# Kernel tuning notes

Hardware: AMD Instinct MI355X
Metric: run time of the kernel (lower is better)

The kernel has to match this reference:

```python
import jax, jax.numpy as jnp
import numpy as np
import math

D_MODEL = 2048
HEADS = 16
D_K = D_MODEL // HEADS  # 128
D_FF = 2048
N = 8192
EPS = 1e-6


def _norm(x, alpha, bias):
    # torch Norm: alpha * (x - mean) / (std + eps) + bias, std uses ddof=1
    mu = jnp.mean(x, axis=-1, keepdims=True)
    sd = jnp.std(x, axis=-1, ddof=1, keepdims=True)
    return alpha * (x - mu) / (sd + EPS) + bias


def setup_inputs() -> dict:
    key = jax.random.key(0)
    ks = jax.random.split(key, 16)
    s = 0.02
    inp = {
        "q": jax.random.normal(ks[0], (N, D_MODEL), jnp.float32),
        "k": jax.random.normal(ks[1], (N, D_MODEL), jnp.float32),
        "v": jax.random.normal(ks[2], (N, D_MODEL), jnp.float32),
        # norm params (norm_1 exists in module but is unused in forward)
        "nq_a": jnp.ones((D_MODEL,), jnp.float32), "nq_b": jnp.zeros((D_MODEL,), jnp.float32),
        "nk_a": jnp.ones((D_MODEL,), jnp.float32), "nk_b": jnp.zeros((D_MODEL,), jnp.float32),
        "nv_a": jnp.ones((D_MODEL,), jnp.float32), "nv_b": jnp.zeros((D_MODEL,), jnp.float32),
        "n2_a": jnp.ones((D_MODEL,), jnp.float32), "n2_b": jnp.zeros((D_MODEL,), jnp.float32),
        # attention projections, stored [in, out]
        "Wq": jax.random.normal(ks[3], (D_MODEL, D_MODEL), jnp.float32) * s,
        "bq": jnp.zeros((D_MODEL,), jnp.float32),
        "Wk": jax.random.normal(ks[4], (D_MODEL, D_MODEL), jnp.float32) * s,
        "bk": jnp.zeros((D_MODEL,), jnp.float32),
        "Wv": jax.random.normal(ks[5], (D_MODEL, D_MODEL), jnp.float32) * s,
        "bv": jnp.zeros((D_MODEL,), jnp.float32),
        "Wo": jax.random.normal(ks[6], (D_MODEL, D_MODEL), jnp.float32) * s,
        "bo": jnp.zeros((D_MODEL,), jnp.float32),
        # FFN
        "W1": jax.random.normal(ks[7], (D_MODEL, D_FF), jnp.float32) * s,
        "b1": jnp.zeros((D_FF,), jnp.float32),
        "W2": jax.random.normal(ks[8], (D_FF, D_MODEL), jnp.float32) * s,
        "b2": jnp.zeros((D_MODEL,), jnp.float32),
    }
    return inp


def reference(q, k, v,
              nq_a, nq_b, nk_a, nk_b, nv_a, nv_b, n2_a, n2_b,
              Wq, bq, Wk, bk, Wv, bv, Wo, bo, W1, b1, W2, b2):
    x = v  # residual stream (dropout is identity at inference)
    qn = _norm(q, nq_a, nq_b)
    kn = _norm(k, nk_a, nk_b)
    vn = _norm(v, nv_a, nv_b)

    # projections -> [N, h, d_k] then transpose(1,2) -> [N, d_k, h]
    qh = (qn @ Wq + bq).reshape(N, HEADS, D_K).transpose(0, 2, 1)
    kh = (kn @ Wk + bk).reshape(N, HEADS, D_K).transpose(0, 2, 1)
    vh = (vn @ Wv + bv).reshape(N, HEADS, D_K).transpose(0, 2, 1)

    # NON-STANDARD (as-written in source): per-token [d_k, d_k] attention
    # contracting over the head axis, scaled by 1/sqrt(d_k).
    scores = jnp.einsum('nah,nbh->nab', qh, kh) / math.sqrt(D_K)  # [N, d_k, d_k]
    probs = jax.nn.softmax(scores, axis=-1)
    attn = jnp.einsum('nab,nbh->nah', probs, vh)  # [N, d_k, h]

    concat = attn.transpose(0, 2, 1).reshape(N, D_MODEL)  # [N, h*d_k]
    x = x + (concat @ Wo + bo)

    x2 = _norm(x, n2_a, n2_b)
    ff = jax.nn.relu(x2 @ W1 + b1) @ W2 + b2
    return x + ff
```

## Files before the change

### kernel.cpp

```cpp
#include <hip/hip_runtime.h>
#include <hip/hip_bf16.h>

#define DM 2048
#define NTOK 8192
#define EPS 1e-6f

typedef __attribute__((ext_vector_type(8))) short short8;
typedef __attribute__((ext_vector_type(4))) short short4v;
typedef __attribute__((ext_vector_type(4))) float f32x4;
typedef __attribute__((ext_vector_type(16))) float f32x16;
typedef __attribute__((ext_vector_type(4))) unsigned int u32x4;

typedef const __attribute__((address_space(1))) void gvoid;
typedef __attribute__((address_space(3))) void lvoid;

static __device__ __forceinline__ unsigned short f2bf(float f) {
    unsigned u = __builtin_bit_cast(unsigned, f);
    unsigned r = u + 0x7FFFu + ((u >> 16) & 1u);
    return (unsigned short)(r >> 16);
}
static __device__ __forceinline__ float bf2f(unsigned short h) {
    return __builtin_bit_cast(float, (unsigned)h << 16);
}

__global__ __launch_bounds__(256) void norm_rows(
        const float* __restrict__ in, const float* __restrict__ alpha,
        const float* __restrict__ beta, unsigned short* __restrict__ out) {
    const int row = blockIdx.x;
    const int t = threadIdx.x;
    const float* x = in + (size_t)row * DM + t * 8;
    float4 v0 = *(const float4*)(x);
    float4 v1 = *(const float4*)(x + 4);
    float s = (v0.x + v0.y) + (v0.z + v0.w) + (v1.x + v1.y) + (v1.z + v1.w);
    float ss = v0.x*v0.x + v0.y*v0.y + v0.z*v0.z + v0.w*v0.w
             + v1.x*v1.x + v1.y*v1.y + v1.z*v1.z + v1.w*v1.w;
    #pragma unroll
    for (int m = 1; m < 64; m <<= 1) {
        s  += __shfl_xor(s, m);
        ss += __shfl_xor(ss, m);
    }
    __shared__ float red[8];
    const int wv = t >> 6, ln = t & 63;
    if (ln == 0) { red[wv] = s; red[4 + wv] = ss; }
    __syncthreads();
    s  = (red[0] + red[1]) + (red[2] + red[3]);
    ss = (red[4] + red[5]) + (red[6] + red[7]);
    const float mu = s * (1.0f / DM);
    float var = (ss - s * mu) * (1.0f / (DM - 1));
    var = fmaxf(var, 0.0f);
    const float scale = 1.0f / (sqrtf(var) + EPS);
    float4 a0 = *(const float4*)(alpha + t*8);
    float4 a1 = *(const float4*)(alpha + t*8 + 4);
    float4 b0 = *(const float4*)(beta + t*8);
    float4 b1 = *(const float4*)(beta + t*8 + 4);
    short8 o;
    o[0] = (short)f2bf(a0.x * (v0.x - mu) * scale + b0.x);
    o[1] = (short)f2bf(a0.y * (v0.y - mu) * scale + b0.y);
    o[2] = (short)f2bf(a0.z * (v0.z - mu) * scale + b0.z);
    o[3] = (short)f2bf(a0.w * (v0.w - mu) * scale + b0.w);
    o[4] = (short)f2bf(a1.x * (v1.x - mu) * scale + b1.x);
    o[5] = (short)f2bf(a1.y * (v1.y - mu) * scale + b1.y);
    o[6] = (short)f2bf(a1.z * (v1.z - mu) * scale + b1.z);
    o[7] = (short)f2bf(a1.w * (v1.w - mu) * scale + b1.w);
    *(short8*)(out + (size_t)row * DM + t * 8) = o;
}

__global__ __launch_bounds__(256) void norm_rows_bf16(
        const unsigned short* __restrict__ in, const float* __restrict__ alpha,
        const float* __restrict__ beta, unsigned short* __restrict__ out) {
    const int row = blockIdx.x;
    const int t = threadIdx.x;
    short8 rv = *(const short8*)(in + (size_t)row * DM + t * 8);
    float xv[8];
    #pragma unroll
    for (int j = 0; j < 8; ++j) xv[j] = bf2f((unsigned short)rv[j]);
    float s = 0.f, ss = 0.f;
    #pragma unroll
    for (int j = 0; j < 8; ++j) { s += xv[j]; ss += xv[j]*xv[j]; }
    #pragma unroll
    for (int m = 1; m < 64; m <<= 1) {
        s  += __shfl_xor(s, m);
        ss += __shfl_xor(ss, m);
    }
    __shared__ float red[8];
    const int wv = t >> 6, ln = t & 63;
    if (ln == 0) { red[wv] = s; red[4 + wv] = ss; }
    __syncthreads();
    s  = (red[0] + red[1]) + (red[2] + red[3]);
    ss = (red[4] + red[5]) + (red[6] + red[7]);
    const float mu = s * (1.0f / DM);
    float var = (ss - s * mu) * (1.0f / (DM - 1));
    var = fmaxf(var, 0.0f);
    const float scale = 1.0f / (sqrtf(var) + EPS);
    short8 o;
    #pragma unroll
    for (int j = 0; j < 8; ++j) {
        const float av = alpha[t*8 + j], bv = beta[t*8 + j];
        o[j] = (short)f2bf(av * (xv[j] - mu) * scale + bv);
    }
    *(short8*)(out + (size_t)row * DM + t * 8) = o;
}

__global__ __launch_bounds__(256) void wtrans(
        const float* __restrict__ W, unsigned short* __restrict__ Wt, int perm, float wscale) {
    __shared__ float tile[32][33];
    const int bc = blockIdx.x * 32, bk = blockIdx.y * 32;
    const int t = threadIdx.x;
    const int tc = t & 31, tr = t >> 5;
    #pragma unroll
    for (int i = 0; i < 4; ++i)
        tile[tr + i*8][tc] = W[(size_t)(bk + tr + i*8) * DM + bc + tc];
    __syncthreads();
    #pragma unroll
    for (int i = 0; i < 4; ++i) {
        const int c = bc + tr + i*8;
        const int pc = perm ? ((c & 127) * 16 + (c >> 7)) : c;
        Wt[(size_t)pc * DM + bk + tc] = f2bf(tile[tc][tr + i*8] * wscale);
    }
}

#define BARRIER __builtin_amdgcn_s_barrier()
#define WAIT_LGKM0 asm volatile("s_waitcnt lgkmcnt(0)" ::: "memory")
#define VMCNT(n) asm volatile("s_waitcnt vmcnt(" #n ")" ::: "memory")

template<int EPI>
__global__ __launch_bounds__(512, 2) void gemm256(
        const unsigned short* __restrict__ A, const unsigned short* __restrict__ Bt,
        const float* __restrict__ bias, const float* __restrict__ residF,
        const unsigned short* __restrict__ residB,
        float* __restrict__ outF, unsigned short* __restrict__ outB, int biasPerm,
        float bscale) {
    __shared__ __align__(16) char lds[131072];
    char* ldsA = lds;
    char* ldsB = lds + 65536;

    const int t = threadIdx.x, l = t & 63, w = t >> 6;
    const int wm = w >> 2, wn = w & 3;

    const int b = blockIdx.x;
    const int xcd = b & 7;
    const int j = b >> 3;
    const int m0 = (xcd * 4 + (j & 3)) * 256;
    const int n0 = (j >> 2) * 256;

    const int rS = t >> 3;
    const int cS = ((t & 7) ^ (rS & 7)) * 8;
    const unsigned short* aSt = A  + (size_t)(m0 + rS) * 2048 + cS;
    const unsigned short* bSt = Bt + (size_t)(n0 + rS) * 2048 + cS;
    const int ldsStW = w * 1024;

    const int aRd = wm * 16384 + (l & 15) * 128;
    const int bRd = (wn >> 1) * 16384 + (wn & 1) * 8192 + (l & 15) * 128;
    const int ch0 = (((l >> 4) + 0) ^ (l & 7)) * 16;
    const int ch1 = (((l >> 4) + 4) ^ (l & 7)) * 16;

    short8 af[4][2], bf[4][2];
    f32x4 acc[8][4] = {};

#define STG_A(buf, h, kt) do { \
    __builtin_amdgcn_global_load_lds((gvoid*)(aSt + (size_t)((h)*128)*2048 + (kt)*64), \
        (lvoid*)(ldsA + (buf)*32768 + (h)*16384 + ldsStW), 16, 0, 0); \
    __builtin_amdgcn_global_load_lds((gvoid*)(aSt + (size_t)((h)*128+64)*2048 + (kt)*64), \
        (lvoid*)(ldsA + (buf)*32768 + (h)*16384 + 8192 + ldsStW), 16, 0, 0); \
} while(0)
#define STG_B(buf, h, kt) do { \
    __builtin_amdgcn_global_load_lds((gvoid*)(bSt + (size_t)((h)*128)*2048 + (kt)*64), \
        (lvoid*)(ldsB + (buf)*32768 + (h)*16384 + ldsStW), 16, 0, 0); \
    __builtin_amdgcn_global_load_lds((gvoid*)(bSt + (size_t)((h)*128+64)*2048 + (kt)*64), \
        (lvoid*)(ldsB + (buf)*32768 + (h)*16384 + 8192 + ldsStW), 16, 0, 0); \
} while(0)
#define RD_A(buf, mh) do { \
    _Pragma("unroll") for (int ml = 0; ml < 4; ++ml) { \
        af[ml][0] = *(const short8*)(ldsA + (buf)*32768 + aRd + ((mh)*4+ml)*2048 + ch0); \
        af[ml][1] = *(const short8*)(ldsA + (buf)*32768 + aRd + ((mh)*4+ml)*2048 + ch1); \
    } } while(0)
#define RD_B(buf, nh) do { \
    _Pragma("unroll") for (int nl = 0; nl < 2; ++nl) { \
        bf[(nh)*2+nl][0] = *(const short8*)(ldsB + (buf)*32768 + bRd + ((nh)*2+nl)*2048 + ch0); \
        bf[(nh)*2+nl][1] = *(const short8*)(ldsB + (buf)*32768 + bRd + ((nh)*2+nl)*2048 + ch1); \
    } } while(0)
#define MM_Q(mh, nh) do { \
    __builtin_amdgcn_s_setprio(1); \
    _Pragma("unroll") for (int ml = 0; ml < 4; ++ml) \
    _Pragma("unroll") for (int nl = 0; nl < 2; ++nl) { \
        acc[(mh)*4+ml][(nh)*2+nl] = __builtin_amdgcn_mfma_f32_16x16x32_bf16( \
            af[ml][0], bf[(nh)*2+nl][0], acc[(mh)*4+ml][(nh)*2+nl], 0, 0, 0); \
        acc[(mh)*4+ml][(nh)*2+nl] = __builtin_amdgcn_mfma_f32_16x16x32_bf16( \
            af[ml][1], bf[(nh)*2+nl][1], acc[(mh)*4+ml][(nh)*2+nl], 0, 0, 0); \
    } \
    __builtin_amdgcn_s_setprio(0); \
} while(0)

    STG_B(0, 0, 0); STG_B(0, 1, 0); STG_A(0, 0, 0); STG_A(0, 1, 0);
    STG_B(1, 0, 1); STG_B(1, 1, 1);
    VMCNT(4);
    BARRIER;

    #pragma unroll 1
    for (int i = 0; i < 16; ++i) {
        const int kt1 = 2*i + 1, k2 = 2*i + 2, k3 = 2*i + 3;
        const bool more = (i < 15);
        RD_A(0, 0); RD_B(0, 0);
        STG_A(1, 0, kt1);
        BARRIER; WAIT_LGKM0;
        MM_Q(0, 0);
        BARRIER;
        RD_B(0, 1);
        STG_A(1, 1, kt1);
        BARRIER; WAIT_LGKM0;
        MM_Q(0, 1);
        BARRIER;
        RD_A(0, 1);
        if (more) STG_B(0, 0, k2);
        BARRIER; WAIT_LGKM0;
        MM_Q(1, 1);
        BARRIER;
        if (more) { STG_B(0, 1, k2); VMCNT(4); } else { VMCNT(0); }
        BARRIER;
        MM_Q(1, 0);
        BARRIER;
        RD_A(1, 0); RD_B(1, 0);
        if (more) STG_A(0, 0, k2);
        BARRIER; WAIT_LGKM0;
        MM_Q(0, 0);
        BARRIER;
        RD_B(1, 1);
        if (more) STG_A(0, 1, k2);
        BARRIER; WAIT_LGKM0;
        MM_Q(0, 1);
        BARRIER;
        RD_A(1, 1);
        if (more) STG_B(1, 0, k3);
        BARRIER; WAIT_LGKM0;
        MM_Q(1, 1);
        BARRIER;
        if (more) { STG_B(1, 1, k3); VMCNT(4); }
        BARRIER;
        MM_Q(1, 0);
        BARRIER;
    }

    #pragma unroll
    for (int ni = 0; ni < 4; ++ni) {
        const int col = n0 + wn*64 + ni*16 + (l & 15);
        const int cb = biasPerm ? ((col >> 4) + (col & 15) * 128) : col;
        const float bvv = bias[cb] * bscale;
        #pragma unroll
        for (int mi = 0; mi < 8; ++mi) {
            #pragma unroll
            for (int r = 0; r < 4; ++r) {
                const int rowg = m0 + wm*128 + mi*16 + (l >> 4)*4 + r;
                float vv = acc[mi][ni][r] + bvv;
                if (EPI == 1) vv = fmaxf(vv, 0.0f);
                const size_t idx = (size_t)rowg * 2048 + col;
                if (EPI == 3)      outB[idx] = f2bf(vv + residF[idx]);
                else if (EPI == 4) outF[idx] = vv + bf2f(residB[idx]);
                else               outB[idx] = f2bf(vv);
            }
        }
    }
#undef STG_A
#undef STG_B
#undef RD_A
#undef RD_B
#undef MM_Q
}

__global__ __launch_bounds__(256) void attn_tok(
        const unsigned short* __restrict__ Qt, const unsigned short* __restrict__ Kt,
        const unsigned short* __restrict__ Vp, unsigned short* __restrict__ Cc) {
    const int n = blockIdx.x;
    const int t = threadIdx.x, w = t >> 6, l = t & 63;
    const int q31 = l & 31, hi = l >> 5;
    __shared__ __align__(16) unsigned short c_s[16 * 132];

    const size_t tb = (size_t)n * DM;
    const short8 qf = *(const short8*)(Qt + tb + (w*32 + q31)*16 + hi*8);
    short8 kf[4];
    #pragma unroll
    for (int bt = 0; bt < 4; ++bt)
        kf[bt] = *(const short8*)(Kt + tb + (bt*32 + q31)*16 + hi*8);
    short8 vf[8];
    #pragma unroll
    for (int ks = 0; ks < 8; ++ks)
        vf[ks] = *(const short8*)(Vp + tb + (q31 & 15)*128 + ks*16 + hi*8);

    const f32x16 z = {};
    f32x16 sc[4];
    #pragma unroll
    for (int bt = 0; bt < 4; ++bt)
        sc[bt] = __builtin_amdgcn_mfma_f32_32x32x16_bf16(kf[bt], qf, z, 0, 0, 0);

    float m0 = sc[0][0], m1 = sc[1][0], m2 = sc[2][0], m3 = sc[3][0];
    #pragma unroll
    for (int r = 1; r < 16; ++r) {
        m0 = fmaxf(m0, sc[0][r]); m1 = fmaxf(m1, sc[1][r]);
        m2 = fmaxf(m2, sc[2][r]); m3 = fmaxf(m3, sc[3][r]);
    }
    float mx = fmaxf(fmaxf(m0, m1), fmaxf(m2, m3));
    { float a2 = mx, b2 = mx;
      asm volatile("v_permlane32_swap_b32 %0, %1" : "+v"(a2), "+v"(b2));
      mx = fmaxf(a2, b2); }

    float p[4][16];
    float s0 = 0.f, s1 = 0.f, s2 = 0.f, s3 = 0.f;
    #pragma unroll
    for (int r = 0; r < 16; ++r) {
        p[0][r] = __expf(sc[0][r] - mx); s0 += p[0][r];
        p[1][r] = __expf(sc[1][r] - mx); s1 += p[1][r];
        p[2][r] = __expf(sc[2][r] - mx); s2 += p[2][r];
        p[3][r] = __expf(sc[3][r] - mx); s3 += p[3][r];
    }
    float sm = (s0 + s1) + (s2 + s3);
    { float a2 = sm, b2 = sm;
      asm volatile("v_permlane32_swap_b32 %0, %1" : "+v"(a2), "+v"(b2));
      sm = a2 + b2; }
    const float inv = __builtin_amdgcn_rcpf(sm);
    #pragma unroll
    for (int bt = 0; bt < 4; ++bt)
        #pragma unroll
        for (int r = 0; r < 16; ++r)
            p[bt][r] *= inv;

    f32x16 acc = {};
    #pragma unroll
    for (int ks = 0; ks < 8; ++ks) {
        const int bt = ks >> 1, r0 = (ks & 1) * 8;
        unsigned X0, Y0, X1, Y1;
        asm("v_cvt_pk_bf16_f32 %0, %1, %2" : "=v"(X0) : "v"(p[bt][r0+0]), "v"(p[bt][r0+1]));
        asm("v_cvt_pk_bf16_f32 %0, %1, %2" : "=v"(Y0) : "v"(p[bt][r0+4]), "v"(p[bt][r0+5]));
        asm("v_cvt_pk_bf16_f32 %0, %1, %2" : "=v"(X1) : "v"(p[bt][r0+2]), "v"(p[bt][r0+3]));
        asm("v_cvt_pk_bf16_f32 %0, %1, %2" : "=v"(Y1) : "v"(p[bt][r0+6]), "v"(p[bt][r0+7]));
        asm volatile("v_permlane32_swap_b32 %0, %1" : "+v"(X0), "+v"(Y0));
        asm volatile("v_permlane32_swap_b32 %0, %1" : "+v"(X1), "+v"(Y1));
        u32x4 pw; pw[0] = X0; pw[1] = X1; pw[2] = Y0; pw[3] = Y1;
        const short8 paf = __builtin_bit_cast(short8, pw);
        acc = __builtin_amdgcn_mfma_f32_32x32x16_bf16(paf, vf[ks], acc, 0, 0, 0);
    }

    if (q31 < 16) {
        #pragma unroll
        for (int rp = 0; rp < 8; ++rp) {
            const int r = rp * 2;
            const int a = (r & 3) + 8 * (r >> 2) + 4 * hi;
            unsigned pk;
            asm("v_cvt_pk_bf16_f32 %0, %1, %2" : "=v"(pk) : "v"(acc[r]), "v"(acc[r+1]));
            *(unsigned*)((char*)c_s + q31*264 + (w*32 + a)*2) = pk;
        }
    }
    __syncthreads();
    *(short8*)(Cc + tb + t*8) = *(const short8*)((char*)c_s + (t >> 4)*264 + (t & 15)*16);
}

extern "C" void kernel_launch(void* const* d_in, const int* in_sizes, int n_in,
                              void* d_out, int out_size, void* d_ws, size_t ws_size,
                              hipStream_t stream) {
    (void)in_sizes; (void)n_in; (void)out_size; (void)ws_size;
    const float* q    = (const float*)d_in[0];
    const float* k    = (const float*)d_in[1];
    const float* v    = (const float*)d_in[2];
    const float* nq_a = (const float*)d_in[3];
    const float* nq_b = (const float*)d_in[4];
    const float* nk_a = (const float*)d_in[5];
    const float* nk_b = (const float*)d_in[6];
    const float* nv_a = (const float*)d_in[7];
    const float* nv_b = (const float*)d_in[8];
    const float* n2_a = (const float*)d_in[9];
    const float* n2_b = (const float*)d_in[10];
    const float* Wq   = (const float*)d_in[11];
    const float* bq   = (const float*)d_in[12];
    const float* Wk   = (const float*)d_in[13];
    const float* bk   = (const float*)d_in[14];
    const float* Wv   = (const float*)d_in[15];
    const float* bv   = (const float*)d_in[16];
    const float* Wo   = (const float*)d_in[17];
    const float* bo   = (const float*)d_in[18];
    const float* W1   = (const float*)d_in[19];
    const float* b1   = (const float*)d_in[20];
    const float* W2   = (const float*)d_in[21];
    const float* b2   = (const float*)d_in[22];

    char* ws = (char*)d_ws;
    const size_t MB = 1024 * 1024;
    unsigned short* buf0 = (unsigned short*)(ws);
    unsigned short* QtB  = (unsigned short*)(ws + 32*MB);
    unsigned short* KtB  = (unsigned short*)(ws + 64*MB);
    unsigned short* VpB  = (unsigned short*)(ws + 96*MB);
    unsigned short* Wqt  = (unsigned short*)(ws + 128*MB);
    unsigned short* Wkt  = (unsigned short*)(ws + 136*MB);
    unsigned short* Wvt  = (unsigned short*)(ws + 144*MB);
    unsigned short* Wot  = (unsigned short*)(ws + 152*MB);
    unsigned short* W1t  = (unsigned short*)(ws + 160*MB);
    unsigned short* W2t  = (unsigned short*)(ws + 168*MB);
    unsigned short* x2   = QtB;
    unsigned short* h1   = KtB;
    unsigned short* xb   = VpB;
    float* x = (float*)d_out;

    const float isq = 0.088388347648318447f;

    dim3 b256(256);
    dim3 gT(DM / 32, DM / 32);
    wtrans<<<gT, b256, 0, stream>>>(Wq, Wqt, 1, isq);
    wtrans<<<gT, b256, 0, stream>>>(Wk, Wkt, 1, 1.0f);
    wtrans<<<gT, b256, 0, stream>>>(Wv, Wvt, 0, 1.0f);
    wtrans<<<gT, b256, 0, stream>>>(Wo, Wot, 0, 1.0f);
    wtrans<<<gT, b256, 0, stream>>>(W1, W1t, 0, 1.0f);
    wtrans<<<gT, b256, 0, stream>>>(W2, W2t, 0, 1.0f);

    dim3 gN(NTOK);
    dim3 gG(256);
    dim3 b512(512);

    norm_rows<<<gN, b256, 0, stream>>>(q, nq_a, nq_b, buf0);
    gemm256<0><<<gG, b512, 0, stream>>>(buf0, Wqt, bq, nullptr, nullptr, nullptr, QtB, 1, isq);
    norm_rows<<<gN, b256, 0, stream>>>(k, nk_a, nk_b, buf0);
    gemm256<0><<<gG, b512, 0, stream>>>(buf0, Wkt, bk, nullptr, nullptr, nullptr, KtB, 1, 1.0f);
    norm_rows<<<gN, b256, 0, stream>>>(v, nv_a, nv_b, buf0);
    gemm256<0><<<gG, b512, 0, stream>>>(buf0, Wvt, bv, nullptr, nullptr, nullptr, VpB, 0, 1.0f);
    attn_tok<<<gN, b256, 0, stream>>>(QtB, KtB, VpB, buf0);
    gemm256<3><<<gG, b512, 0, stream>>>(buf0, Wot, bo, v, nullptr, nullptr, xb, 0, 1.0f);
    norm_rows_bf16<<<gN, b256, 0, stream>>>(xb, n2_a, n2_b, x2);
    gemm256<1><<<gG, b512, 0, stream>>>(x2, W1t, b1, nullptr, nullptr, nullptr, h1, 0, 1.0f);
    gemm256<4><<<gG, b512, 0, stream>>>(h1, W2t, b2, nullptr, xb, x, nullptr, 0, 1.0f);
}
```

Before: 598.8 us.

## Stage GEMM epilogue through LDS, restructure prefetch, batch weight transposes

The GEMM epilogue now writes bias-added bf16 results into LDS in two passes, then reads them back as 16-byte row segments for coalesced vector global stores and residual loads. Scalar per-element stores spread across strided rows go away. The K-loop prefetch now issues a whole A/B stage up front and groups the stage loads differently, waiting on a deeper vmcnt. The six weight-transpose launches are merged into one launch using blockIdx.z. The tradeoff is extra LDS round trips and barriers in the epilogue, plus an intermediate bf16 rounding before the residual add.

```diff
diff --git a/kernel.cpp b/kernel.cpp
--- a/kernel.cpp
+++ b/kernel.cpp
@@ -101,9 +101,20 @@
     *(short8*)(out + (size_t)row * DM + t * 8) = o;
 }
 
-__global__ __launch_bounds__(256) void wtrans(
-        const float* __restrict__ W, unsigned short* __restrict__ Wt, int perm, float wscale) {
+__global__ __launch_bounds__(256) void wtrans6(
+        const float* __restrict__ Wq, const float* __restrict__ Wk,
+        const float* __restrict__ Wv, const float* __restrict__ Wo,
+        const float* __restrict__ W1, const float* __restrict__ W2,
+        unsigned short* __restrict__ Tq, unsigned short* __restrict__ Tk,
+        unsigned short* __restrict__ Tv, unsigned short* __restrict__ To,
+        unsigned short* __restrict__ T1, unsigned short* __restrict__ T2,
+        float isq) {
     __shared__ float tile[32][33];
+    const int z = blockIdx.z;
+    const float* W = z==0?Wq: z==1?Wk: z==2?Wv: z==3?Wo: z==4?W1: W2;
+    unsigned short* Wt = z==0?Tq: z==1?Tk: z==2?Tv: z==3?To: z==4?T1: T2;
+    const int perm = (z < 2) ? 1 : 0;
+    const float ws = (z == 0) ? isq : 1.0f;
     const int bc = blockIdx.x * 32, bk = blockIdx.y * 32;
     const int t = threadIdx.x;
     const int tc = t & 31, tr = t >> 5;
@@ -115,7 +126,7 @@
     for (int i = 0; i < 4; ++i) {
         const int c = bc + tr + i*8;
         const int pc = perm ? ((c & 127) * 16 + (c >> 7)) : c;
-        Wt[(size_t)pc * DM + bk + tc] = f2bf(tile[tc][tr + i*8] * wscale);
+        Wt[(size_t)pc * DM + bk + tc] = f2bf(tile[tc][tr + i*8] * ws);
     }
 }
 
@@ -192,70 +203,109 @@
 } while(0)
 
     STG_B(0, 0, 0); STG_B(0, 1, 0); STG_A(0, 0, 0); STG_A(0, 1, 0);
-    STG_B(1, 0, 1); STG_B(1, 1, 1);
-    VMCNT(4);
+    STG_B(1, 0, 1); STG_B(1, 1, 1); STG_A(1, 0, 1); STG_A(1, 1, 1);
+    VMCNT(8);
     BARRIER;
 
     #pragma unroll 1
     for (int i = 0; i < 16; ++i) {
-        const int kt1 = 2*i + 1, k2 = 2*i + 2, k3 = 2*i + 3;
+        const int k2 = 2*i + 2, k3 = 2*i + 3;
         const bool more = (i < 15);
         RD_A(0, 0); RD_B(0, 0);
-        STG_A(1, 0, kt1);
         BARRIER; WAIT_LGKM0;
         MM_Q(0, 0);
         BARRIER;
         RD_B(0, 1);
-        STG_A(1, 1, kt1);
         BARRIER; WAIT_LGKM0;
         MM_Q(0, 1);
         BARRIER;
         RD_A(0, 1);
-        if (more) STG_B(0, 0, k2);
+        if (more) { STG_B(0, 0, k2); STG_B(0, 1, k2); }
         BARRIER; WAIT_LGKM0;
         MM_Q(1, 1);
         BARRIER;
-        if (more) { STG_B(0, 1, k2); VMCNT(4); } else { VMCNT(0); }
+        if (more) { STG_A(0, 0, k2); STG_A(0, 1, k2); VMCNT(8); } else { VMCNT(0); }
         BARRIER;
         MM_Q(1, 0);
         BARRIER;
         RD_A(1, 0); RD_B(1, 0);
-        if (more) STG_A(0, 0, k2);
         BARRIER; WAIT_LGKM0;
         MM_Q(0, 0);
         BARRIER;
         RD_B(1, 1);
-        if (more) STG_A(0, 1, k2);
         BARRIER; WAIT_LGKM0;
         MM_Q(0, 1);
         BARRIER;
         RD_A(1, 1);
-        if (more) STG_B(1, 0, k3);
+        if (more) { STG_B(1, 0, k3); STG_B(1, 1, k3); }
         BARRIER; WAIT_LGKM0;
         MM_Q(1, 1);
         BARRIER;
-        if (more) { STG_B(1, 1, k3); VMCNT(4); }
+        if (more) { STG_A(1, 0, k3); STG_A(1, 1, k3); VMCNT(8); } else { VMCNT(0); }
         BARRIER;
         MM_Q(1, 0);
         BARRIER;
     }
 
-    #pragma unroll
-    for (int ni = 0; ni < 4; ++ni) {
-        const int col = n0 + wn*64 + ni*16 + (l & 15);
-        const int cb = biasPerm ? ((col >> 4) + (col & 15) * 128) : col;
-        const float bvv = bias[cb] * bscale;
+    unsigned short* cs = (unsigned short*)lds;
+    #pragma unroll 1
+    for (int pass = 0; pass < 2; ++pass) {
+        BARRIER;
+        if (wm == pass) {
+            #pragma unroll
+            for (int ni = 0; ni < 4; ++ni) {
+                const int col = wn*64 + ni*16 + (l & 15);
+                const int gcol = n0 + col;
+                const int cb = biasPerm ? ((gcol >> 4) + (gcol & 15) * 128) : gcol;
+                const float bvv = bias[cb] * bscale;
+                #pragma unroll
+                for (int mi = 0; mi < 8; ++mi) {
+                    #pragma unroll
+                    for (int r = 0; r < 4; ++r) {
+                        const int row = mi*16 + (l >> 4)*4 + r;
+                        float vv = acc[mi][ni][r] + bvv;
+                        if (EPI == 1) vv = fmaxf(vv, 0.0f);
+                        cs[row*260 + col] = f2bf(vv);
+                    }
+                }
+            }
+        }
+        BARRIER;
         #pragma unroll
-        for (int mi = 0; mi < 8; ++mi) {
-            #pragma unroll
-            for (int r = 0; r < 4; ++r) {
-                const int rowg = m0 + wm*128 + mi*16 + (l >> 4)*4 + r;
-                float vv = acc[mi][ni][r] + bvv;
-                if (EPI == 1) vv = fmaxf(vv, 0.0f);
-                const size_t idx = (size_t)rowg * 2048 + col;
-                if (EPI == 3)      outB[idx] = f2bf(vv + residF[idx]);
-                else if (EPI == 4) outF[idx] = vv + bf2f(residB[idx]);
-                else               outB[idx] = f2bf(vv);
+        for (int s = 0; s < 8; ++s) {
+            const int row = (t >> 5) + s*16;
+            const int seg = t & 31;
+            short8 pk = *(const short8*)(cs + row*260 + seg*8);
+            const int grow = m0 + pass*128 + row;
+            const size_t gb = (size_t)grow * 2048 + n0 + seg*8;
+            if (EPI == 3) {
+                float4 r0 = *(const float4*)(residF + gb);
+                float4 r1 = *(const float4*)(residF + gb + 4);
+                short8 o;
+                o[0] = (short)f2bf(bf2f((unsigned short)pk[0]) + r0.x);
+                o[1] = (short)f2bf(bf2f((unsigned short)pk[1]) + r0.y);
+                o[2] = (short)f2bf(bf2f((unsigned short)pk[2]) + r0.z);
+                o[3] = (short)f2bf(bf2f((unsigned short)pk[3]) + r0.w);
+                o[4] = (short)f2bf(bf2f((unsigned short)pk[4]) + r1.x);
+                o[5] = (short)f2bf(bf2f((unsigned short)pk[5]) + r1.y);
+                o[6] = (short)f2bf(bf2f((unsigned short)pk[6]) + r1.z);
+                o[7] = (short)f2bf(bf2f((unsigned short)pk[7]) + r1.w);
+                *(short8*)(outB + gb) = o;
+            } else if (EPI == 4) {
+                short8 rb = *(const short8*)(residB + gb);
+                float4 o0, o1;
+                o0.x = bf2f((unsigned short)pk[0]) + bf2f((unsigned short)rb[0]);
+                o0.y = bf2f((unsigned short)pk[1]) + bf2f((unsigned short)rb[1]);
+                o0.z = bf2f((unsigned short)pk[2]) + bf2f((unsigned short)rb[2]);
+                o0.w = bf2f((unsigned short)pk[3]) + bf2f((unsigned short)rb[3]);
+                o1.x = bf2f((unsigned short)pk[4]) + bf2f((unsigned short)rb[4]);
+                o1.y = bf2f((unsigned short)pk[5]) + bf2f((unsigned short)rb[5]);
+                o1.z = bf2f((unsigned short)pk[6]) + bf2f((unsigned short)rb[6]);
+                o1.w = bf2f((unsigned short)pk[7]) + bf2f((unsigned short)rb[7]);
+                *(float4*)(outF + gb) = o0;
+                *(float4*)(outF + gb + 4) = o1;
+            } else {
+                *(short8*)(outB + gb) = pk;
             }
         }
     }
@@ -400,13 +450,9 @@
     const float isq = 0.088388347648318447f;
 
     dim3 b256(256);
-    dim3 gT(DM / 32, DM / 32);
-    wtrans<<<gT, b256, 0, stream>>>(Wq, Wqt, 1, isq);
-    wtrans<<<gT, b256, 0, stream>>>(Wk, Wkt, 1, 1.0f);
-    wtrans<<<gT, b256, 0, stream>>>(Wv, Wvt, 0, 1.0f);
-    wtrans<<<gT, b256, 0, stream>>>(Wo, Wot, 0, 1.0f);
-    wtrans<<<gT, b256, 0, stream>>>(W1, W1t, 0, 1.0f);
-    wtrans<<<gT, b256, 0, stream>>>(W2, W2t, 0, 1.0f);
+    dim3 gT6(DM / 32, DM / 32, 6);
+    wtrans6<<<gT6, b256, 0, stream>>>(Wq, Wk, Wv, Wo, W1, W2,
+                                      Wqt, Wkt, Wvt, Wot, W1t, W2t, isq);
 
     dim3 gN(NTOK);
     dim3 gG(256);
```

New measurement: 579.7 us. 1.03x faster.
